# Kernel tuning notes

Measured on AMD Instinct MI355X. Metric: run time of the kernel, lower is better.

The kernel has to match this reference:

```python
import jax, jax.numpy as jnp
import numpy as np

N_NODES = 100000
N_EDGES = 640000
D_IN = 128
EPS = 1e-12  # torch F.normalize eps


def _sage_conv(x, src, dst, Wl, Wr, b):
    # mean aggregation of neighbor features: for each dst node, mean of x[src]
    n = x.shape[0]
    agg = jax.ops.segment_sum(x[src], dst, num_segments=n)
    cnt = jax.ops.segment_sum(jnp.ones((src.shape[0],), x.dtype), dst, num_segments=n)
    agg = agg / jnp.maximum(cnt, 1.0)[:, None]
    # out = lin_l(agg) + lin_r(x); PyG puts bias in lin_l
    h = agg @ Wl.T + b + x @ Wr.T
    # normalize=True -> L2 normalize rows
    norm = jnp.linalg.norm(h, axis=-1, keepdims=True)
    return h / jnp.maximum(norm, EPS)


def setup_inputs() -> dict:
    key = jax.random.key(0)
    ks = jax.random.split(key, 12)
    hid = 256
    inp = {
        "x": jax.random.normal(ks[0], (N_NODES, D_IN), dtype=jnp.float32),
        "edge_index": jax.random.randint(ks[1], (2, N_EDGES), 0, N_NODES, dtype=jnp.int64),
        "W1l": jax.random.normal(ks[2], (hid, D_IN), dtype=jnp.float32) * 0.05,
        "W1r": jax.random.normal(ks[3], (hid, D_IN), dtype=jnp.float32) * 0.05,
        "b1": jax.random.normal(ks[4], (hid,), dtype=jnp.float32) * 0.05,
        "W2l": jax.random.normal(ks[5], (hid // 2, hid), dtype=jnp.float32) * 0.05,
        "W2r": jax.random.normal(ks[6], (hid // 2, hid), dtype=jnp.float32) * 0.05,
        "b2": jax.random.normal(ks[7], (hid // 2,), dtype=jnp.float32) * 0.05,
        "W3l": jax.random.normal(ks[8], (2, hid // 2), dtype=jnp.float32) * 0.05,
        "W3r": jax.random.normal(ks[9], (2, hid // 2), dtype=jnp.float32) * 0.05,
        "b3": jax.random.normal(ks[10], (2,), dtype=jnp.float32) * 0.05,
    }
    return inp


def reference(x, edge_index, W1l, W1r, b1, W2l, W2r, b2, W3l, W3r, b3):
    src, dst = edge_index[0], edge_index[1]
    h = _sage_conv(x, src, dst, W1l, W1r, b1)
    h = jax.nn.relu(h)  # dropout is identity in eval mode
    h = _sage_conv(h, src, dst, W2l, W2r, b2)
    h = jax.nn.relu(h)
    h = _sage_conv(h, src, dst, W3l, W3r, b3)
    return jax.nn.log_softmax(h, axis=1)
```

## Files before the change

### kernel.cpp

```cpp
#include <hip/hip_runtime.h>
#include <math.h>

#define NN 100000
#define NE 640000
#define NBLK 98
#define GBLK 1563

typedef __bf16 bf16_t;
typedef bf16_t bf16x8 __attribute__((ext_vector_type(8)));
typedef float  f32x4  __attribute__((ext_vector_type(4)));


__global__ __launch_bounds__(256) void k_hist(const int* __restrict__ dst,
                                              int* __restrict__ deg) {
    int e = blockIdx.x * 256 + threadIdx.x;
    if (e < NE) atomicAdd(&deg[dst[e]], 1);
}

__global__ __launch_bounds__(1024) void k_bsum(const int* __restrict__ deg,
                                               int* __restrict__ bsum) {
    __shared__ int warr[16];
    int t = threadIdx.x;
    int i = blockIdx.x * 1024 + t;
    int v = (i < NN) ? deg[i] : 0;
    int lane = t & 63, wid = t >> 6;
    #pragma unroll
    for (int off = 32; off > 0; off >>= 1) v += __shfl_xor(v, off, 64);
    if (lane == 0) warr[wid] = v;
    __syncthreads();
    if (t < 16) {
        int s = warr[t];
        #pragma unroll
        for (int off = 8; off > 0; off >>= 1) s += __shfl_xor(s, off, 64);
        if (t == 0) bsum[blockIdx.x] = s;
    }
}

__global__ __launch_bounds__(64) void k_bscan(const int* __restrict__ bsum,
        int* __restrict__ boff, int* __restrict__ rowptr) {
    int lane = threadIdx.x;
    int carry = 0;
    for (int base = 0; base < NBLK; base += 64) {
        int i = base + lane;
        int v = (i < NBLK) ? bsum[i] : 0;
        int s = v;
        #pragma unroll
        for (int off = 1; off < 64; off <<= 1) {
            int u = __shfl_up(s, off, 64);
            if (lane >= off) s += u;
        }
        if (i < NBLK) boff[i] = carry + s - v;
        carry += __shfl(s, 63, 64);
    }
    if (lane == 0) rowptr[NN] = NE;
}

__global__ __launch_bounds__(1024) void k_scan2(const int* __restrict__ deg,
        const int* __restrict__ boff, int* __restrict__ rowptr,
        int* __restrict__ cursor) {
    __shared__ int wsum[16];
    __shared__ int woff[16];
    int t = threadIdx.x;
    int lane = t & 63, wid = t >> 6;
    int i = blockIdx.x * 1024 + t;
    int v = (i < NN) ? deg[i] : 0;
    int s = v;
    #pragma unroll
    for (int off = 1; off < 64; off <<= 1) {
        int u = __shfl_up(s, off, 64);
        if (lane >= off) s += u;
    }
    if (lane == 63) wsum[wid] = s;
    __syncthreads();
    if (wid == 0) {
        int ws = (lane < 16) ? wsum[lane] : 0;
        #pragma unroll
        for (int off = 1; off < 16; off <<= 1) {
            int u = __shfl_up(ws, off, 64);
            if (lane >= off) ws += u;
        }
        if (lane < 16) woff[lane] = ws;
    }
    __syncthreads();
    if (i < NN) {
        int excl = boff[blockIdx.x] + (s - v) + (wid ? woff[wid - 1] : 0);
        rowptr[i] = excl;
        cursor[i] = excl;
    }
}

__global__ __launch_bounds__(256) void k_fill(const int* __restrict__ src,
        const int* __restrict__ dst, int* __restrict__ cursor,
        int* __restrict__ csr) {
    int e = blockIdx.x * 256 + threadIdx.x;
    if (e >= NE) return;
    int p = atomicAdd(&cursor[dst[e]], 1);
    csr[p] = src[e];
}


__global__ __launch_bounds__(256) void k_split_w(const float* __restrict__ W1l,
        const float* __restrict__ W1r, const float* __restrict__ W2l,
        const float* __restrict__ W2r, bf16_t* __restrict__ W1fh,
        bf16_t* __restrict__ W1fl, bf16_t* __restrict__ W2fh,
        bf16_t* __restrict__ W2fl) {
    int b = blockIdx.x, t = threadIdx.x;
    float f;
    bf16_t* Wfh;
    bf16_t* Wfl;
    int j;
    if (b < 256) {
        j = b;
        f = (t < 128) ? W1l[j * 128 + t] : W1r[j * 128 + (t - 128)];
        Wfh = W1fh; Wfl = W1fl;
    } else {
        j = b - 256;
        f = (j < 128) ? W2l[j * 256 + t] : W2r[(j - 128) * 256 + t];
        Wfh = W2fh; Wfl = W2fl;
    }
    bf16_t h = (bf16_t)f;
    bf16_t l = (bf16_t)(f - (float)h);
    int idx = (((j >> 4) * 8 + (t >> 5)) * 64 + ((t >> 3) & 3) * 16 + (j & 15)) * 8 + (t & 7);
    Wfh[idx] = h;
    Wfl[idx] = l;
}


__global__ __launch_bounds__(256) void k_gather128s(const float* __restrict__ feat,
        const int* __restrict__ rowptr, const int* __restrict__ csr,
        float* __restrict__ agg) {
    int tid = blockIdx.x * 256 + threadIdx.x;
    int node = tid >> 5;
    if (node >= NN) return;
    int lane4 = (tid & 31) << 2;
    int beg = rowptr[node], end = rowptr[node + 1];
    float4 acc = make_float4(0.f, 0.f, 0.f, 0.f);
    int e = beg;
    for (; e + 1 < end; e += 2) {
        int s0 = csr[e], s1 = csr[e + 1];
        float4 v0 = *(const float4*)(feat + (size_t)s0 * 128 + lane4);
        float4 v1 = *(const float4*)(feat + (size_t)s1 * 128 + lane4);
        acc.x += v0.x + v1.x; acc.y += v0.y + v1.y;
        acc.z += v0.z + v1.z; acc.w += v0.w + v1.w;
    }
    if (e < end) {
        int s0 = csr[e];
        float4 v0 = *(const float4*)(feat + (size_t)s0 * 128 + lane4);
        acc.x += v0.x; acc.y += v0.y; acc.z += v0.z; acc.w += v0.w;
    }
    float iv = 1.0f / (float)max(end - beg, 1);
    acc.x *= iv; acc.y *= iv; acc.z *= iv; acc.w *= iv;
    *(float4*)(agg + (size_t)node * 128 + lane4) = acc;
}


__device__ __forceinline__ void splitv(float4 v0, float4 v1,
                                       bf16x8& h, bf16x8& l) {
    float f[8] = {v0.x, v0.y, v0.z, v0.w, v1.x, v1.y, v1.z, v1.w};
    #pragma unroll
    for (int i = 0; i < 8; i++) {
        bf16_t hi = (bf16_t)f[i];
        h[i] = hi;
        l[i] = (bf16_t)(f[i] - (float)hi);
    }
}

__global__ __launch_bounds__(256, 2) void k_gemm_fused(const float* __restrict__ Aa,
        const float* __restrict__ Ax, const bf16_t* __restrict__ W1fh,
        const bf16_t* __restrict__ W1fl, const bf16_t* __restrict__ W2fh,
        const bf16_t* __restrict__ W2fl, const float* __restrict__ bias,
        float* __restrict__ C2) {
    __shared__ bf16_t sHf[64 * 256], sLf[64 * 256];
    __shared__ float pr[64][4];
    int t = threadIdx.x;
    int wave = t >> 6, lane = t & 63, quad = lane >> 4, l16 = lane & 15;
    int r0 = blockIdx.x * 64;
    int arow = t >> 2, aseg = t & 3;
    int grow = r0 + arow; if (grow >= NN) grow = NN - 1;
    #pragma unroll
    for (int it = 0; it < 8; it++) {
        int k0 = it * 32;
        const float* Asrc = (k0 < 128) ? Aa : Ax;
        int kb = (k0 < 128) ? k0 : (k0 - 128);
        const float* p = &Asrc[(size_t)grow * 128 + kb + aseg * 8];
        bf16x8 h8, l8;
        splitv(*(const float4*)p, *(const float4*)(p + 4), h8, l8);
        int idx = (((arow >> 4) * 8 + it) * 64 + aseg * 16 + (arow & 15)) * 8;
        *(bf16x8*)&sHf[idx] = h8;
        *(bf16x8*)&sLf[idx] = l8;
    }
    __syncthreads();
    f32x4 acc[4][4] = {};
    for (int it = 0; it < 8; it++) {
        bf16x8 bh[4], bl[4];
        #pragma unroll
        for (int nt = 0; nt < 4; nt++) {
            size_t fo = (size_t)(((wave * 4 + nt) * 8 + it) * 64 + lane) * 8;
            bh[nt] = *(const bf16x8*)&W1fh[fo];
            bl[nt] = *(const bf16x8*)&W1fl[fo];
        }
        #pragma unroll
        for (int mt = 0; mt < 4; mt++) {
            int fb = ((mt * 8 + it) * 64 + lane) * 8;
            bf16x8 ah = *(bf16x8*)&sHf[fb];
            bf16x8 al = *(bf16x8*)&sLf[fb];
            #pragma unroll
            for (int nt = 0; nt < 4; nt++) {
                acc[mt][nt] = __builtin_amdgcn_mfma_f32_16x16x32_bf16(ah, bh[nt], acc[mt][nt], 0, 0, 0);
                acc[mt][nt] = __builtin_amdgcn_mfma_f32_16x16x32_bf16(al, bh[nt], acc[mt][nt], 0, 0, 0);
                acc[mt][nt] = __builtin_amdgcn_mfma_f32_16x16x32_bf16(ah, bl[nt], acc[mt][nt], 0, 0, 0);
            }
        }
    }
    float bcol[4];
    #pragma unroll
    for (int nt = 0; nt < 4; nt++) bcol[nt] = bias[wave * 64 + nt * 16 + l16];
    #pragma unroll
    for (int mt = 0; mt < 4; mt++)
        #pragma unroll
        for (int nt = 0; nt < 4; nt++)
            #pragma unroll
            for (int rg = 0; rg < 4; rg++)
                acc[mt][nt][rg] += bcol[nt];
    float ss[4][4];
    #pragma unroll
    for (int mt = 0; mt < 4; mt++)
        #pragma unroll
        for (int rg = 0; rg < 4; rg++) {
            float s = 0.f;
            #pragma unroll
            for (int nt = 0; nt < 4; nt++) s += acc[mt][nt][rg] * acc[mt][nt][rg];
            #pragma unroll
            for (int off = 1; off < 16; off <<= 1) s += __shfl_xor(s, off, 64);
            ss[mt][rg] = s;
        }
    if (l16 == 0) {
        #pragma unroll
        for (int mt = 0; mt < 4; mt++)
            #pragma unroll
            for (int rg = 0; rg < 4; rg++)
                pr[mt * 16 + quad * 4 + rg][wave] = ss[mt][rg];
    }
    __syncthreads();
    #pragma unroll
    for (int mt = 0; mt < 4; mt++)
        #pragma unroll
        for (int rg = 0; rg < 4; rg++) {
            int r = mt * 16 + quad * 4 + rg;
            float tot = pr[r][0] + pr[r][1] + pr[r][2] + pr[r][3];
            float inv = 1.0f / fmaxf(sqrtf(tot), 1e-12f);
            #pragma unroll
            for (int nt = 0; nt < 4; nt++) {
                int c = wave * 64 + nt * 16 + l16;
                float v = fmaxf(acc[mt][nt][rg] * inv, 0.f);
                bf16_t h = (bf16_t)v;
                bf16_t l = (bf16_t)(v - (float)h);
                int idx = (((r >> 4) * 8 + (c >> 5)) * 64 + ((c >> 3) & 3) * 16 + (r & 15)) * 8 + (c & 7);
                sHf[idx] = h;
                sLf[idx] = l;
            }
        }
    __syncthreads();
    f32x4 acc2[4][4] = {};
    for (int it = 0; it < 8; it++) {
        bf16x8 bh[4], bl[4];
        #pragma unroll
        for (int nt = 0; nt < 4; nt++) {
            size_t fo = (size_t)(((wave * 4 + nt) * 8 + it) * 64 + lane) * 8;
            bh[nt] = *(const bf16x8*)&W2fh[fo];
            bl[nt] = *(const bf16x8*)&W2fl[fo];
        }
        #pragma unroll
        for (int mt = 0; mt < 4; mt++) {
            int fb = ((mt * 8 + it) * 64 + lane) * 8;
            bf16x8 ah = *(bf16x8*)&sHf[fb];
            bf16x8 al = *(bf16x8*)&sLf[fb];
            #pragma unroll
            for (int nt = 0; nt < 4; nt++) {
                acc2[mt][nt] = __builtin_amdgcn_mfma_f32_16x16x32_bf16(ah, bh[nt], acc2[mt][nt], 0, 0, 0);
                acc2[mt][nt] = __builtin_amdgcn_mfma_f32_16x16x32_bf16(al, bh[nt], acc2[mt][nt], 0, 0, 0);
                acc2[mt][nt] = __builtin_amdgcn_mfma_f32_16x16x32_bf16(ah, bl[nt], acc2[mt][nt], 0, 0, 0);
            }
        }
    }
    #pragma unroll
    for (int mt = 0; mt < 4; mt++)
        #pragma unroll
        for (int rg = 0; rg < 4; rg++) {
            int row = r0 + mt * 16 + quad * 4 + rg;
            if (row >= NN) continue;
            #pragma unroll
            for (int nt = 0; nt < 4; nt++) {
                int col = wave * 64 + nt * 16 + l16;
                C2[(size_t)row * 256 + col] = acc2[mt][nt][rg];
            }
        }
}


__global__ __launch_bounds__(256) void k_gather_combine(const float* __restrict__ C2,
        const int* __restrict__ rowptr, const int* __restrict__ csr,
        const float* __restrict__ b2, const float* __restrict__ W3l,
        float* __restrict__ h2, float* __restrict__ q3) {
    __shared__ float sw[256];
    int t = threadIdx.x;
    sw[t] = W3l[t];
    __syncthreads();
    int tid = blockIdx.x * 256 + t;
    int node = tid >> 5;
    if (node >= NN) return;
    int l = tid & 31;
    int lane4 = l << 2;
    int beg = rowptr[node], end = rowptr[node + 1];
    float4 acc = make_float4(0.f, 0.f, 0.f, 0.f);
    int e = beg;
    for (; e + 1 < end; e += 2) {
        int s0 = csr[e], s1 = csr[e + 1];
        float4 v0 = *(const float4*)(C2 + (size_t)s0 * 256 + lane4);
        float4 v1 = *(const float4*)(C2 + (size_t)s1 * 256 + lane4);
        acc.x += v0.x + v1.x; acc.y += v0.y + v1.y;
        acc.z += v0.z + v1.z; acc.w += v0.w + v1.w;
    }
    if (e < end) {
        int s0 = csr[e];
        float4 v0 = *(const float4*)(C2 + (size_t)s0 * 256 + lane4);
        acc.x += v0.x; acc.y += v0.y; acc.z += v0.z; acc.w += v0.w;
    }
    float iv = 1.0f / (float)max(end - beg, 1);
    float4 r = *(const float4*)&C2[(size_t)node * 256 + 128 + lane4];
    float4 b = *(const float4*)&b2[lane4];
    float v0 = acc.x * iv + r.x + b.x;
    float v1 = acc.y * iv + r.y + b.y;
    float v2 = acc.z * iv + r.z + b.z;
    float v3 = acc.w * iv + r.w + b.w;
    float s = v0 * v0 + v1 * v1 + v2 * v2 + v3 * v3;
    #pragma unroll
    for (int off = 16; off > 0; off >>= 1) s += __shfl_xor(s, off, 64);
    float invn = 1.0f / fmaxf(sqrtf(s), 1e-12f);
    float4 o;
    o.x = fmaxf(v0 * invn, 0.f); o.y = fmaxf(v1 * invn, 0.f);
    o.z = fmaxf(v2 * invn, 0.f); o.w = fmaxf(v3 * invn, 0.f);
    *(float4*)&h2[(size_t)node * 128 + lane4] = o;
    float a0 = o.x * sw[lane4] + o.y * sw[lane4+1] + o.z * sw[lane4+2] + o.w * sw[lane4+3];
    float a1 = o.x * sw[128+lane4] + o.y * sw[129+lane4] + o.z * sw[130+lane4] + o.w * sw[131+lane4];
    #pragma unroll
    for (int off = 16; off > 0; off >>= 1) {
        a0 += __shfl_xor(a0, off, 64);
        a1 += __shfl_xor(a1, off, 64);
    }
    if (l == 0) {
        q3[2 * node] = a0;
        q3[2 * node + 1] = a1;
    }
}


__global__ __launch_bounds__(256) void k_final(const float* __restrict__ h2,
        const float* __restrict__ W3r, const float* __restrict__ b3,
        const float* __restrict__ q3, const int* __restrict__ rowptr,
        const int* __restrict__ csr, float* __restrict__ out) {
    __shared__ float sw[256];
    int t = threadIdx.x;
    sw[t] = W3r[t];
    __syncthreads();
    int i = blockIdx.x * 256 + t;
    if (i >= NN) return;
    int beg = rowptr[i], end = rowptr[i + 1];
    float g0 = 0.f, g1 = 0.f;
    for (int e = beg; e < end; e++) {
        int s = csr[e];
        g0 += q3[2 * s];
        g1 += q3[2 * s + 1];
    }
    float ivd = 1.0f / (float)max(end - beg, 1);
    g0 *= ivd; g1 *= ivd;
    const float4* row = (const float4*)(h2 + (size_t)i * 128);
    float a0 = 0.f, a1 = 0.f;
    #pragma unroll
    for (int q = 0; q < 32; q++) {
        float4 v = row[q];
        a0 += v.x * sw[4*q] + v.y * sw[4*q+1] + v.z * sw[4*q+2] + v.w * sw[4*q+3];
        a1 += v.x * sw[128+4*q] + v.y * sw[129+4*q] + v.z * sw[130+4*q] + v.w * sw[131+4*q];
    }
    float v0 = g0 + a0 + b3[0];
    float v1 = g1 + a1 + b3[1];
    float invn = 1.0f / fmaxf(sqrtf(v0 * v0 + v1 * v1), 1e-12f);
    v0 *= invn; v1 *= invn;
    float mx = fmaxf(v0, v1);
    float l = logf(expf(v0 - mx) + expf(v1 - mx));
    out[2 * i] = v0 - mx - l;
    out[2 * i + 1] = v1 - mx - l;
}


extern "C" void kernel_launch(void* const* d_in, const int* in_sizes, int n_in,
                              void* d_out, int out_size, void* d_ws, size_t ws_size,
                              hipStream_t stream) {
    const float* x   = (const float*)d_in[0];
    const int*   ei  = (const int*)d_in[1];
    const float* W1l = (const float*)d_in[2];
    const float* W1r = (const float*)d_in[3];
    const float* b1  = (const float*)d_in[4];
    const float* W2l = (const float*)d_in[5];
    const float* W2r = (const float*)d_in[6];
    const float* b2  = (const float*)d_in[7];
    const float* W3l = (const float*)d_in[8];
    const float* W3r = (const float*)d_in[9];
    const float* b3  = (const float*)d_in[10];
    float* out = (float*)d_out;
    const int* src = ei;
    const int* dst = ei + NE;

    int* deg    = (int*)d_ws;
    int* rowptr = deg + 102400;
    int* cursor = rowptr + 102400;
    int* csr    = cursor + 102400;
    int* bsum   = csr + 655360;
    int* boff   = bsum + 128;
    bf16_t* W1h  = (bf16_t*)(boff + 128);
    bf16_t* W1lo = W1h + 65536;
    bf16_t* W2h  = W1lo + 65536;
    bf16_t* W2lo = W2h + 65536;
    float* aggA = (float*)(W2lo + 65536);
    float* C2   = aggA + 12800000;
    float* h2   = C2 + (size_t)GBLK * 64 * 256;
    float* q3   = h2 + 12800000;

    hipMemsetAsync(deg, 0, NN * sizeof(int), stream);
    k_hist<<<(NE + 255) / 256, 256, 0, stream>>>(dst, deg);
    k_bsum<<<NBLK, 1024, 0, stream>>>(deg, bsum);
    k_bscan<<<1, 64, 0, stream>>>(bsum, boff, rowptr);
    k_scan2<<<NBLK, 1024, 0, stream>>>(deg, boff, rowptr, cursor);
    k_fill<<<(NE + 255) / 256, 256, 0, stream>>>(src, dst, cursor, csr);

    k_split_w<<<512, 256, 0, stream>>>(W1l, W1r, W2l, W2r, W1h, W1lo, W2h, W2lo);

    k_gather128s<<<(NN * 32 + 255) / 256, 256, 0, stream>>>(x, rowptr, csr, aggA);

    k_gemm_fused<<<GBLK, 256, 0, stream>>>(aggA, x, W1h, W1lo, W2h, W2lo, b1, C2);

    k_gather_combine<<<(NN * 32 + 255) / 256, 256, 0, stream>>>(C2, rowptr, csr, b2, W3l, h2, q3);

    k_final<<<(NN + 255) / 256, 256, 0, stream>>>(h2, W3r, b3, q3, rowptr, csr, out);
}
```

Before: 396.3 us.

## Fuse layer-1 neighbor mean aggregation into the GEMM prologue and split C2 output

The separate gather kernel that wrote the aggregated layer-1 features to global memory is removed. The fused GEMM kernel now computes each row's neighbor mean directly into the shared-memory A tile, with 4 threads per row each looping over all edges. The C2 output is split into two contiguous 128-wide buffers so the layer-2 gather reads denser rows. This removes a kernel launch and a 51MB write and read, but the in-GEMM gather uses only 4 threads per row, which lowers memory parallelism and adds load imbalance inside the GEMM blocks.

```diff
diff --git a/kernel.cpp b/kernel.cpp
--- a/kernel.cpp
+++ b/kernel.cpp
@@ -126,34 +126,6 @@
 }
 
 
-__global__ __launch_bounds__(256) void k_gather128s(const float* __restrict__ feat,
-        const int* __restrict__ rowptr, const int* __restrict__ csr,
-        float* __restrict__ agg) {
-    int tid = blockIdx.x * 256 + threadIdx.x;
-    int node = tid >> 5;
-    if (node >= NN) return;
-    int lane4 = (tid & 31) << 2;
-    int beg = rowptr[node], end = rowptr[node + 1];
-    float4 acc = make_float4(0.f, 0.f, 0.f, 0.f);
-    int e = beg;
-    for (; e + 1 < end; e += 2) {
-        int s0 = csr[e], s1 = csr[e + 1];
-        float4 v0 = *(const float4*)(feat + (size_t)s0 * 128 + lane4);
-        float4 v1 = *(const float4*)(feat + (size_t)s1 * 128 + lane4);
-        acc.x += v0.x + v1.x; acc.y += v0.y + v1.y;
-        acc.z += v0.z + v1.z; acc.w += v0.w + v1.w;
-    }
-    if (e < end) {
-        int s0 = csr[e];
-        float4 v0 = *(const float4*)(feat + (size_t)s0 * 128 + lane4);
-        acc.x += v0.x; acc.y += v0.y; acc.z += v0.z; acc.w += v0.w;
-    }
-    float iv = 1.0f / (float)max(end - beg, 1);
-    acc.x *= iv; acc.y *= iv; acc.z *= iv; acc.w *= iv;
-    *(float4*)(agg + (size_t)node * 128 + lane4) = acc;
-}
-
-
 __device__ __forceinline__ void splitv(float4 v0, float4 v1,
                                        bf16x8& h, bf16x8& l) {
     float f[8] = {v0.x, v0.y, v0.z, v0.w, v1.x, v1.y, v1.z, v1.w};
@@ -165,11 +137,12 @@
     }
 }
 
-__global__ __launch_bounds__(256, 2) void k_gemm_fused(const float* __restrict__ Aa,
-        const float* __restrict__ Ax, const bf16_t* __restrict__ W1fh,
-        const bf16_t* __restrict__ W1fl, const bf16_t* __restrict__ W2fh,
-        const bf16_t* __restrict__ W2fl, const float* __restrict__ bias,
-        float* __restrict__ C2) {
+__global__ __launch_bounds__(256, 2) void k_gemm_fused(const float* __restrict__ Ax,
+        const int* __restrict__ rowptr, const int* __restrict__ csr,
+        const bf16_t* __restrict__ W1fh, const bf16_t* __restrict__ W1fl,
+        const bf16_t* __restrict__ W2fh, const bf16_t* __restrict__ W2fl,
+        const float* __restrict__ bias,
+        float* __restrict__ C2a, float* __restrict__ C2r) {
     __shared__ bf16_t sHf[64 * 256], sLf[64 * 256];
     __shared__ float pr[64][4];
     int t = threadIdx.x;
@@ -177,12 +150,42 @@
     int r0 = blockIdx.x * 64;
     int arow = t >> 2, aseg = t & 3;
     int grow = r0 + arow; if (grow >= NN) grow = NN - 1;
-    #pragma unroll
-    for (int it = 0; it < 8; it++) {
-        int k0 = it * 32;
-        const float* Asrc = (k0 < 128) ? Aa : Ax;
-        int kb = (k0 < 128) ? k0 : (k0 - 128);
-        const float* p = &Asrc[(size_t)grow * 128 + kb + aseg * 8];
+    {
+        int beg = rowptr[grow], end = rowptr[grow + 1];
+        float iv = 1.0f / (float)max(end - beg, 1);
+        f32x4 ac[8] = {};
+        for (int e = beg; e < end; e++) {
+            int s = csr[e];
+            const float* prow = &Ax[(size_t)s * 128 + aseg * 8];
+            #pragma unroll
+            for (int it = 0; it < 4; it++) {
+                ac[it * 2]     += *(const f32x4*)(prow + it * 32);
+                ac[it * 2 + 1] += *(const f32x4*)(prow + it * 32 + 4);
+            }
+        }
+        #pragma unroll
+        for (int it = 0; it < 4; it++) {
+            f32x4 v0 = ac[it * 2] * iv;
+            f32x4 v1 = ac[it * 2 + 1] * iv;
+            bf16x8 h8, l8;
+            #pragma unroll
+            for (int i = 0; i < 4; i++) {
+                bf16_t hh = (bf16_t)v0[i];
+                h8[i] = hh; l8[i] = (bf16_t)(v0[i] - (float)hh);
+            }
+            #pragma unroll
+            for (int i = 0; i < 4; i++) {
+                bf16_t hh = (bf16_t)v1[i];
+                h8[i + 4] = hh; l8[i + 4] = (bf16_t)(v1[i] - (float)hh);
+            }
+            int idx = (((arow >> 4) * 8 + it) * 64 + aseg * 16 + (arow & 15)) * 8;
+            *(bf16x8*)&sHf[idx] = h8;
+            *(bf16x8*)&sLf[idx] = l8;
+        }
+    }
+    #pragma unroll
+    for (int it = 4; it < 8; it++) {
+        const float* p = &Ax[(size_t)grow * 128 + (it - 4) * 32 + aseg * 8];
         bf16x8 h8, l8;
         splitv(*(const float4*)p, *(const float4*)(p + 4), h8, l8);
         int idx = (((arow >> 4) * 8 + it) * 64 + aseg * 16 + (arow & 15)) * 8;
@@ -283,6 +286,8 @@
             }
         }
     }
+    float* dstb = (wave < 2) ? C2a : C2r;
+    int cb = (wave < 2) ? (wave * 64) : ((wave - 2) * 64);
     #pragma unroll
     for (int mt = 0; mt < 4; mt++)
         #pragma unroll
@@ -291,14 +296,15 @@
             if (row >= NN) continue;
             #pragma unroll
             for (int nt = 0; nt < 4; nt++) {
-                int col = wave * 64 + nt * 16 + l16;
-                C2[(size_t)row * 256 + col] = acc2[mt][nt][rg];
-            }
-        }
-}
-
-
-__global__ __launch_bounds__(256) void k_gather_combine(const float* __restrict__ C2,
+                int col = cb + nt * 16 + l16;
+                dstb[(size_t)row * 128 + col] = acc2[mt][nt][rg];
+            }
+        }
+}
+
+
+__global__ __launch_bounds__(256) void k_gather_combine(const float* __restrict__ C2a,
+        const float* __restrict__ C2r,
         const int* __restrict__ rowptr, const int* __restrict__ csr,
         const float* __restrict__ b2, const float* __restrict__ W3l,
         float* __restrict__ h2, float* __restrict__ q3) {
@@ -316,18 +322,18 @@
     int e = beg;
     for (; e + 1 < end; e += 2) {
         int s0 = csr[e], s1 = csr[e + 1];
-        float4 v0 = *(const float4*)(C2 + (size_t)s0 * 256 + lane4);
-        float4 v1 = *(const float4*)(C2 + (size_t)s1 * 256 + lane4);
+        float4 v0 = *(const float4*)(C2a + (size_t)s0 * 128 + lane4);
+        float4 v1 = *(const float4*)(C2a + (size_t)s1 * 128 + lane4);
         acc.x += v0.x + v1.x; acc.y += v0.y + v1.y;
         acc.z += v0.z + v1.z; acc.w += v0.w + v1.w;
     }
     if (e < end) {
         int s0 = csr[e];
-        float4 v0 = *(const float4*)(C2 + (size_t)s0 * 256 + lane4);
+        float4 v0 = *(const float4*)(C2a + (size_t)s0 * 128 + lane4);
         acc.x += v0.x; acc.y += v0.y; acc.z += v0.z; acc.w += v0.w;
     }
     float iv = 1.0f / (float)max(end - beg, 1);
-    float4 r = *(const float4*)&C2[(size_t)node * 256 + 128 + lane4];
+    float4 r = *(const float4*)&C2r[(size_t)node * 128 + lane4];
     float4 b = *(const float4*)&b2[lane4];
     float v0 = acc.x * iv + r.x + b.x;
     float v1 = acc.y * iv + r.y + b.y;
@@ -421,9 +427,9 @@
     bf16_t* W1lo = W1h + 65536;
     bf16_t* W2h  = W1lo + 65536;
     bf16_t* W2lo = W2h + 65536;
-    float* aggA = (float*)(W2lo + 65536);
-    float* C2   = aggA + 12800000;
-    float* h2   = C2 + (size_t)GBLK * 64 * 256;
+    float* C2a  = (float*)(W2lo + 65536);
+    float* C2r  = C2a + (size_t)GBLK * 64 * 128;
+    float* h2   = C2r + (size_t)GBLK * 64 * 128;
     float* q3   = h2 + 12800000;
 
     hipMemsetAsync(deg, 0, NN * sizeof(int), stream);
@@ -435,11 +441,9 @@
 
     k_split_w<<<512, 256, 0, stream>>>(W1l, W1r, W2l, W2r, W1h, W1lo, W2h, W2lo);
 
-    k_gather128s<<<(NN * 32 + 255) / 256, 256, 0, stream>>>(x, rowptr, csr, aggA);
-
-    k_gemm_fused<<<GBLK, 256, 0, stream>>>(aggA, x, W1h, W1lo, W2h, W2lo, b1, C2);
-
-    k_gather_combine<<<(NN * 32 + 255) / 256, 256, 0, stream>>>(C2, rowptr, csr, b2, W3l, h2, q3);
+    k_gemm_fused<<<GBLK, 256, 0, stream>>>(x, rowptr, csr, W1h, W1lo, W2h, W2lo, b1, C2a, C2r);
+
+    k_gather_combine<<<(NN * 32 + 255) / 256, 256, 0, stream>>>(C2a, C2r, rowptr, csr, b2, W3l, h2, q3);
 
     k_final<<<(NN + 255) / 256, 256, 0, stream>>>(h2, W3r, b3, q3, rowptr, csr, out);
 }
```

Measured after the change: 379.5 us. -4.3%, faster.
